# Kernel optimization log

Hardware: AMD Instinct MI355X
Metric: run time of the kernel (lower is better)

## Reference

```python
import jax, jax.numpy as jnp
import numpy as np

N = 100000
E = 3200000
F_IN = 512
H = 16
C = 40


def gcn_conv(x, edge_index, W, b, num_nodes):
    """PyG GCNConv: y = D^{-1/2} (A + I) D^{-1/2} (x @ W) + b.
    edge_index: [2, E] int, row=source, col=target; self-loops added here."""
    # transform first (small hidden dim keeps message traffic low)
    h = x @ W  # [N, out]
    loops = jnp.arange(num_nodes, dtype=edge_index.dtype)
    row = jnp.concatenate([edge_index[0], loops])
    col = jnp.concatenate([edge_index[1], loops])
    deg = jax.ops.segment_sum(jnp.ones_like(col, dtype=h.dtype), col,
                              num_segments=num_nodes)  # in-degree incl. self-loop
    dinv = jnp.where(deg > 0, jax.lax.rsqrt(deg), 0.0)
    norm = dinv[row] * dinv[col]  # [E+N]
    msgs = h[row] * norm[:, None]  # gather + scale, [E+N, out]
    out = jax.ops.segment_sum(msgs, col, num_segments=num_nodes)  # scatter-add
    return out + b


def setup_inputs() -> dict:
    key = jax.random.key(0)
    k1, k2, k3, k4, k5, k6 = jax.random.split(key, 6)
    x = jax.random.normal(k1, (N, F_IN), dtype=jnp.float32)
    edge_index = jax.random.randint(k2, (2, E), 0, N, dtype=jnp.int64)
    s1 = 1.0 / np.sqrt(F_IN)
    s2 = 1.0 / np.sqrt(H)
    W1 = jax.random.uniform(k3, (F_IN, H), jnp.float32, -s1, s1)
    b1 = jnp.zeros((H,), jnp.float32)
    W2 = jax.random.uniform(k4, (H, C), jnp.float32, -s2, s2)
    b2 = jnp.zeros((C,), jnp.float32)
    return {"x": x, "edge_index": edge_index, "W1": W1, "b1": b1,
            "W2": W2, "b2": b2}


def reference(x, edge_index, W1, b1, W2, b2):
    h = gcn_conv(x, edge_index, W1, b1, N)
    h = jax.nn.relu(h)
    # F.dropout(training=self.training): inference mode -> identity
    h = gcn_conv(h, edge_index, W2, b2, N)
    return jax.nn.log_softmax(h, axis=1)
```

## Files before the change

### kernel.cpp

```cpp
#include <hip/hip_runtime.h>

#define NN 100000
#define EE 3200000
#define FIN 512
#define HH 16
#define CC 40

#define SHIFT 9
#define BNODES 512
#define NB 196
#define CAP 20480
#define CH 2048
#define TC ((EE + CH - 1) / CH)
#define GB2 ((NN + 63) / 64)

__device__ __forceinline__ float bf2f(unsigned short u) {
    return __uint_as_float(((unsigned)u) << 16);
}
__device__ __forceinline__ unsigned short f2bf(float f) {
    unsigned b = __float_as_uint(f);
    return (unsigned short)((b + 0x7FFF + ((b >> 16) & 1)) >> 16);
}

__global__ void k_bin(const int* __restrict__ ei, int* __restrict__ head,
                      int* __restrict__ deg, unsigned* __restrict__ pairs) {
    __shared__ int h[NB];
    __shared__ int gbase[NB];
    __shared__ int lhead[NB];
    __shared__ unsigned esrc[CH];
    __shared__ unsigned edst[CH];
    __shared__ int is64_s;
    int t = threadIdx.x;
    if (t < 64) {
        int nz = (ei[2 * t + 1] != 0) ? 1 : 0;
        unsigned long long m = __ballot(nz);
        if (t == 0) is64_s = (m == 0ULL) ? 1 : 0;
    }
    for (int i = t; i < NB; i += 256) { h[i] = 0; lhead[i] = 0; }
    __syncthreads();
    int is64 = is64_s;
    int e0 = blockIdx.x * CH, e1 = min(EE, e0 + CH);
    for (int e = e0 + t; e < e1; e += 256) {
        int src = is64 ? ei[2 * e] : ei[e];
        int dst = is64 ? ei[2 * (EE + e)] : ei[EE + e];
        esrc[e - e0] = (unsigned)src;
        edst[e - e0] = (unsigned)dst;
        atomicAdd(&h[dst >> SHIFT], 1);
        atomicAdd(&deg[dst], 1);
    }
    __syncthreads();
    for (int i = t; i < NB; i += 256)
        gbase[i] = h[i] ? atomicAdd(&head[i], h[i]) : 0;
    __syncthreads();
    int n = e1 - e0;
    for (int j = t; j < n; j += 256) {
        unsigned src = esrc[j];
        unsigned dst = edst[j];
        int b = (int)(dst >> SHIFT);
        int p = gbase[b] + atomicAdd(&lhead[b], 1);
        pairs[(size_t)b * CAP + p] = ((dst & (BNODES - 1)) << 17) | src;
    }
}

__global__ void __launch_bounds__(256) k_buildgemm(
        const unsigned* __restrict__ pairs, const int* __restrict__ head,
        int* __restrict__ ptr, int* __restrict__ pend,
        float* __restrict__ dinv, int* __restrict__ srcs,
        const float* __restrict__ x, const float* __restrict__ W1,
        const int* __restrict__ deg, unsigned short* __restrict__ g1) {
    __shared__ float red[4][64][17];
    int t = threadIdx.x;
    if (blockIdx.x < NB) {
        int* h   = (int*)red;
        int* lex = (int*)red + BNODES;
        int* wsm = (int*)red + 2 * BNODES;
        int b = blockIdx.x, lane = t & 63, wid = t >> 6;
        int node0 = b << SHIFT;
        int p0 = b * CAP;
        int cnt = head[b];
        for (int i = t; i < BNODES; i += 256) h[i] = 0;
        __syncthreads();
        for (int p = t; p < cnt; p += 256) atomicAdd(&h[pairs[p0 + p] >> 17], 1);
        __syncthreads();
        int a0 = h[2 * t], a1 = h[2 * t + 1];
        int s = a0 + a1;
        int v = s;
#pragma unroll
        for (int off = 1; off < 64; off <<= 1) {
            int u = __shfl_up(v, off);
            if (lane >= off) v += u;
        }
        if (lane == 63) wsm[wid] = v;
        __syncthreads();
        int add = 0;
        for (int w = 0; w < wid; ++w) add += wsm[w];
        int incl = v + add;
        int e0 = incl - s;
        lex[2 * t] = e0;
        lex[2 * t + 1] = e0 + a0;
        __syncthreads();
        for (int i = t; i < BNODES; i += 256) {
            int n = node0 + i;
            if (n < NN) {
                int st = p0 + lex[i];
                ptr[n] = st;
                pend[n] = st + h[i];
                dinv[n] = rsqrtf((float)(h[i] + 1));
            }
        }
        __syncthreads();
        for (int p = t; p < cnt; p += 256) {
            unsigned w = pairs[p0 + p];
            int pos = p0 + atomicAdd(&lex[w >> 17], 1);
            srcs[pos] = (int)(w & 0x1FFFF);
        }
    } else {
        int kq = __builtin_amdgcn_readfirstlane(t >> 6);
        int n = t & 63;
        int base = (blockIdx.x - NB) * 64;
        int nc = min(base + n, NN - 1);
        const float4* xr = reinterpret_cast<const float4*>(
            x + (size_t)nc * FIN + kq * 128);
        const float* wb = W1 + kq * 128 * HH;
        float acc[HH];
#pragma unroll
        for (int f = 0; f < HH; ++f) acc[f] = 0.f;
#pragma unroll 2
        for (int i = 0; i < 32; ++i) {
            float4 xv = xr[i];
            const float* wr = wb + i * 4 * HH;
#pragma unroll
            for (int f = 0; f < HH; ++f) acc[f] = fmaf(xv.x, wr[f], acc[f]);
#pragma unroll
            for (int f = 0; f < HH; ++f) acc[f] = fmaf(xv.y, wr[HH + f], acc[f]);
#pragma unroll
            for (int f = 0; f < HH; ++f) acc[f] = fmaf(xv.z, wr[2 * HH + f], acc[f]);
#pragma unroll
            for (int f = 0; f < HH; ++f) acc[f] = fmaf(xv.w, wr[3 * HH + f], acc[f]);
        }
#pragma unroll
        for (int f = 0; f < HH; ++f) red[kq][n][f] = acc[f];
        __syncthreads();
        int g = t >> 6;
        int f0 = g * 4;
        float r0 = red[0][n][f0]     + red[1][n][f0]     + red[2][n][f0]     + red[3][n][f0];
        float r1 = red[0][n][f0 + 1] + red[1][n][f0 + 1] + red[2][n][f0 + 1] + red[3][n][f0 + 1];
        float r2 = red[0][n][f0 + 2] + red[1][n][f0 + 2] + red[2][n][f0 + 2] + red[3][n][f0 + 2];
        float r3 = red[0][n][f0 + 3] + red[1][n][f0 + 3] + red[2][n][f0 + 3] + red[3][n][f0 + 3];
        int node = base + n;
        if (node < NN) {
            float di = rsqrtf((float)(deg[node] + 1));
            ushort4 o;
            o.x = f2bf(r0 * di);
            o.y = f2bf(r1 * di);
            o.z = f2bf(r2 * di);
            o.w = f2bf(r3 * di);
            reinterpret_cast<ushort4*>(g1)[node * 4 + g] = o;
        }
    }
}

__global__ void k_agg1(const unsigned short* __restrict__ g1, const int* __restrict__ ptr,
                       const int* __restrict__ pend, const int* __restrict__ srcs,
                       const float* __restrict__ dinv, const float* __restrict__ b1,
                       unsigned short* __restrict__ g2h) {
    int gt = blockIdx.x * blockDim.x + threadIdx.x;
    int node = gt >> 2, q = gt & 3;
    if (node >= NN) return;
    const ushort4* G = reinterpret_cast<const ushort4*>(g1);
    ushort4 sv = G[node * 4 + q];
    float ax = bf2f(sv.x), ay = bf2f(sv.y), az = bf2f(sv.z), aw = bf2f(sv.w);
    float bx = 0.f, by = 0.f, bz = 0.f, bw = 0.f;
    float cx = 0.f, cy = 0.f, cz = 0.f, cw = 0.f;
    float dx = 0.f, dy = 0.f, dz = 0.f, dw = 0.f;
    int e = ptr[node], e1 = pend[node];
    for (; e + 3 < e1; e += 4) {
        int s0 = srcs[e], s1 = srcs[e + 1], s2 = srcs[e + 2], s3 = srcs[e + 3];
        ushort4 v0 = G[s0 * 4 + q];
        ushort4 v1 = G[s1 * 4 + q];
        ushort4 v2 = G[s2 * 4 + q];
        ushort4 v3 = G[s3 * 4 + q];
        ax += bf2f(v0.x); ay += bf2f(v0.y); az += bf2f(v0.z); aw += bf2f(v0.w);
        bx += bf2f(v1.x); by += bf2f(v1.y); bz += bf2f(v1.z); bw += bf2f(v1.w);
        cx += bf2f(v2.x); cy += bf2f(v2.y); cz += bf2f(v2.z); cw += bf2f(v2.w);
        dx += bf2f(v3.x); dy += bf2f(v3.y); dz += bf2f(v3.z); dw += bf2f(v3.w);
    }
    for (; e < e1; ++e) {
        ushort4 v = G[srcs[e] * 4 + q];
        ax += bf2f(v.x); ay += bf2f(v.y); az += bf2f(v.z); aw += bf2f(v.w);
    }
    ax += bx + cx + dx;
    ay += by + cy + dy;
    az += bz + cz + dz;
    aw += bw + cw + dw;
    float di = dinv[node];
    const float4 bb = reinterpret_cast<const float4*>(b1)[q];
    ushort4 r;
    r.x = f2bf(fmaxf(fmaf(di, ax, bb.x), 0.f) * di);
    r.y = f2bf(fmaxf(fmaf(di, ay, bb.y), 0.f) * di);
    r.z = f2bf(fmaxf(fmaf(di, az, bb.z), 0.f) * di);
    r.w = f2bf(fmaxf(fmaf(di, aw, bb.w), 0.f) * di);
    reinterpret_cast<ushort4*>(g2h)[node * 4 + q] = r;
}

__global__ void __launch_bounds__(256) k_agg2out(
        const unsigned short* __restrict__ g2h, const int* __restrict__ ptr,
        const int* __restrict__ pend, const int* __restrict__ srcs,
        const float* __restrict__ dinv, const float* __restrict__ W2,
        const float* __restrict__ b2, float* __restrict__ out) {
    __shared__ float w2s[HH * 41];
    __shared__ float b2s[CC];
    int t = threadIdx.x;
    for (int i = t; i < HH * CC; i += 256) w2s[(i / CC) * 41 + (i % CC)] = W2[i];
    if (t < CC) b2s[t] = b2[t];
    __syncthreads();
    int gt = blockIdx.x * blockDim.x + t;
    int node = gt >> 2, q = gt & 3;
    if (node >= NN) return;
    const ushort4* G = reinterpret_cast<const ushort4*>(g2h);
    ushort4 sv = G[node * 4 + q];
    float ax = bf2f(sv.x), ay = bf2f(sv.y), az = bf2f(sv.z), aw = bf2f(sv.w);
    float bx = 0.f, by = 0.f, bz = 0.f, bw = 0.f;
    float cx = 0.f, cy = 0.f, cz = 0.f, cw = 0.f;
    float dx = 0.f, dy = 0.f, dz = 0.f, dw = 0.f;
    int e = ptr[node], e1 = pend[node];
    for (; e + 3 < e1; e += 4) {
        int s0 = srcs[e], s1 = srcs[e + 1], s2 = srcs[e + 2], s3 = srcs[e + 3];
        ushort4 v0 = G[s0 * 4 + q];
        ushort4 v1 = G[s1 * 4 + q];
        ushort4 v2 = G[s2 * 4 + q];
        ushort4 v3 = G[s3 * 4 + q];
        ax += bf2f(v0.x); ay += bf2f(v0.y); az += bf2f(v0.z); aw += bf2f(v0.w);
        bx += bf2f(v1.x); by += bf2f(v1.y); bz += bf2f(v1.z); bw += bf2f(v1.w);
        cx += bf2f(v2.x); cy += bf2f(v2.y); cz += bf2f(v2.z); cw += bf2f(v2.w);
        dx += bf2f(v3.x); dy += bf2f(v3.y); dz += bf2f(v3.z); dw += bf2f(v3.w);
    }
    for (; e < e1; ++e) {
        ushort4 v = G[srcs[e] * 4 + q];
        ax += bf2f(v.x); ay += bf2f(v.y); az += bf2f(v.z); aw += bf2f(v.w);
    }
    ax += bx + cx + dx;
    ay += by + cy + dy;
    az += bz + cz + dz;
    aw += bw + cw + dw;
    const float* w0 = w2s + (4 * q + 0) * 41;
    const float* w1 = w2s + (4 * q + 1) * 41;
    const float* w2r = w2s + (4 * q + 2) * 41;
    const float* w3 = w2s + (4 * q + 3) * 41;
    float y[CC];
#pragma unroll
    for (int c = 0; c < CC; ++c)
        y[c] = fmaf(ax, w0[c], fmaf(ay, w1[c], fmaf(az, w2r[c], aw * w3[c])));
#pragma unroll
    for (int c = 0; c < CC; ++c) {
        y[c] += __shfl_xor(y[c], 1);
        y[c] += __shfl_xor(y[c], 2);
    }
    float di = dinv[node];
    float m = -3.0e38f;
#pragma unroll
    for (int c = 0; c < CC; ++c) {
        y[c] = fmaf(di, y[c], b2s[c]);
        m = fmaxf(m, y[c]);
    }
    float ssum = 0.f;
#pragma unroll
    for (int c = 0; c < CC; ++c) ssum += expf(y[c] - m);
    float l = logf(ssum) + m;
    float ov[10];
#pragma unroll
    for (int c = 0; c < CC; ++c) {
        if ((c / 10) == q) ov[c % 10] = y[c] - l;
    }
    float2* o2 = reinterpret_cast<float2*>(out + (size_t)node * CC + 10 * q);
#pragma unroll
    for (int i = 0; i < 5; ++i) o2[i] = make_float2(ov[2 * i], ov[2 * i + 1]);
}

extern "C" void kernel_launch(void* const* d_in, const int* in_sizes, int n_in,
                              void* d_out, int out_size, void* d_ws, size_t ws_size,
                              hipStream_t stream) {
    const float* x  = (const float*)d_in[0];
    const int*   ei = (const int*)d_in[1];
    const float* W1 = (const float*)d_in[2];
    const float* b1 = (const float*)d_in[3];
    const float* W2 = (const float*)d_in[4];
    const float* b2 = (const float*)d_in[5];
    float* out = (float*)d_out;

    char* w = (char*)d_ws;
    auto alloc = [&](size_t bytes) {
        char* p = w;
        w += (bytes + 255) & ~(size_t)255;
        return p;
    };
    int*            head  = (int*)alloc((size_t)(NB + NN) * 4);
    int*            deg   = head + NB;
    int*            ptr   = (int*)alloc((size_t)NN * 4);
    int*            pend  = (int*)alloc((size_t)NN * 4);
    float*          dinv  = (float*)alloc((size_t)NN * 4);
    unsigned*       pairs = (unsigned*)alloc((size_t)NB * CAP * 4);
    int*            srcs  = (int*)alloc((size_t)NB * CAP * 4);
    unsigned short* g1    = (unsigned short*)alloc((size_t)NN * HH * 2);
    unsigned short* g2h   = (unsigned short*)alloc((size_t)NN * HH * 2);

    hipMemsetAsync(head, 0, (size_t)(NB + NN) * sizeof(int), stream);
    k_bin<<<TC, 256, 0, stream>>>(ei, head, deg, pairs);
    k_buildgemm<<<NB + GB2, 256, 0, stream>>>(pairs, head, ptr, pend, dinv, srcs,
                                              x, W1, deg, g1);
    int nt = NN * 4;
    k_agg1<<<(nt + 255) / 256, 256, 0, stream>>>(g1, ptr, pend, srcs, dinv, b1, g2h);
    k_agg2out<<<(nt + 255) / 256, 256, 0, stream>>>(g2h, ptr, pend, srcs, dinv,
                                                    W2, b2, out);
}
```

Before: 570.6 us.

## Drop global degree atomics in binning; scale GEMM output in separate pass

Removes the per-edge global atomicAdd on the degree array from the binning kernel, relying on dinv computed from the per-bucket histograms in the build kernel. Edge endpoints are kept in registers instead of shared memory staging. Because dinv is only available after the build phase, the GEMM now writes unscaled fp32 results and a new small kernel applies dinv and converts to bf16. This trades 3.2M scattered global atomics and a large memset for an extra 6.4MB write, a re-read of that buffer, and one extra launch.

```diff
diff --git a/kernel.cpp b/kernel.cpp
--- a/kernel.cpp
+++ b/kernel.cpp
@@ -12,6 +12,7 @@
 #define CAP 20480
 #define CH 2048
 #define TC ((EE + CH - 1) / CH)
+#define GB ((NN * 4 + 255) / 256)
 #define GB2 ((NN + 63) / 64)
 
 __device__ __forceinline__ float bf2f(unsigned short u) {
@@ -23,12 +24,10 @@
 }
 
 __global__ void k_bin(const int* __restrict__ ei, int* __restrict__ head,
-                      int* __restrict__ deg, unsigned* __restrict__ pairs) {
+                      unsigned* __restrict__ pairs) {
     __shared__ int h[NB];
     __shared__ int gbase[NB];
     __shared__ int lhead[NB];
-    __shared__ unsigned esrc[CH];
-    __shared__ unsigned edst[CH];
     __shared__ int is64_s;
     int t = threadIdx.x;
     if (t < 64) {
@@ -39,26 +38,29 @@
     for (int i = t; i < NB; i += 256) { h[i] = 0; lhead[i] = 0; }
     __syncthreads();
     int is64 = is64_s;
-    int e0 = blockIdx.x * CH, e1 = min(EE, e0 + CH);
-    for (int e = e0 + t; e < e1; e += 256) {
-        int src = is64 ? ei[2 * e] : ei[e];
-        int dst = is64 ? ei[2 * (EE + e)] : ei[EE + e];
-        esrc[e - e0] = (unsigned)src;
-        edst[e - e0] = (unsigned)dst;
-        atomicAdd(&h[dst >> SHIFT], 1);
-        atomicAdd(&deg[dst], 1);
+    int e0 = blockIdx.x * CH;
+    unsigned es[8], ed[8];
+#pragma unroll
+    for (int j = 0; j < 8; ++j) {
+        int e = e0 + j * 256 + t;
+        if (e < EE) {
+            es[j] = (unsigned)(is64 ? ei[2 * e] : ei[e]);
+            ed[j] = (unsigned)(is64 ? ei[2 * (EE + e)] : ei[EE + e]);
+            atomicAdd(&h[ed[j] >> SHIFT], 1);
+        }
     }
     __syncthreads();
     for (int i = t; i < NB; i += 256)
         gbase[i] = h[i] ? atomicAdd(&head[i], h[i]) : 0;
     __syncthreads();
-    int n = e1 - e0;
-    for (int j = t; j < n; j += 256) {
-        unsigned src = esrc[j];
-        unsigned dst = edst[j];
-        int b = (int)(dst >> SHIFT);
-        int p = gbase[b] + atomicAdd(&lhead[b], 1);
-        pairs[(size_t)b * CAP + p] = ((dst & (BNODES - 1)) << 17) | src;
+#pragma unroll
+    for (int j = 0; j < 8; ++j) {
+        int e = e0 + j * 256 + t;
+        if (e < EE) {
+            int b = (int)(ed[j] >> SHIFT);
+            int p = gbase[b] + atomicAdd(&lhead[b], 1);
+            pairs[(size_t)b * CAP + p] = ((ed[j] & (BNODES - 1)) << 17) | es[j];
+        }
     }
 }
 
@@ -67,7 +69,7 @@
         int* __restrict__ ptr, int* __restrict__ pend,
         float* __restrict__ dinv, int* __restrict__ srcs,
         const float* __restrict__ x, const float* __restrict__ W1,
-        const int* __restrict__ deg, unsigned short* __restrict__ g1) {
+        float* __restrict__ g1f) {
     __shared__ float red[4][64][17];
     int t = threadIdx.x;
     if (blockIdx.x < NB) {
@@ -148,16 +150,25 @@
         float r2 = red[0][n][f0 + 2] + red[1][n][f0 + 2] + red[2][n][f0 + 2] + red[3][n][f0 + 2];
         float r3 = red[0][n][f0 + 3] + red[1][n][f0 + 3] + red[2][n][f0 + 3] + red[3][n][f0 + 3];
         int node = base + n;
-        if (node < NN) {
-            float di = rsqrtf((float)(deg[node] + 1));
-            ushort4 o;
-            o.x = f2bf(r0 * di);
-            o.y = f2bf(r1 * di);
-            o.z = f2bf(r2 * di);
-            o.w = f2bf(r3 * di);
-            reinterpret_cast<ushort4*>(g1)[node * 4 + g] = o;
-        }
-    }
+        if (node < NN)
+            reinterpret_cast<float4*>(g1f)[node * 4 + g] =
+                make_float4(r0, r1, r2, r3);
+    }
+}
+
+__global__ void k_scale(const float* __restrict__ g1f, const float* __restrict__ dinv,
+                        unsigned short* __restrict__ g1) {
+    int gt = blockIdx.x * 256 + threadIdx.x;
+    int node = gt >> 2, q = gt & 3;
+    if (node >= NN) return;
+    float di = dinv[node];
+    float4 v = reinterpret_cast<const float4*>(g1f)[node * 4 + q];
+    ushort4 o;
+    o.x = f2bf(v.x * di);
+    o.y = f2bf(v.y * di);
+    o.z = f2bf(v.z * di);
+    o.w = f2bf(v.w * di);
+    reinterpret_cast<ushort4*>(g1)[node * 4 + q] = o;
 }
 
 __global__ void k_agg1(const unsigned short* __restrict__ g1, const int* __restrict__ ptr,
@@ -294,20 +305,21 @@
         w += (bytes + 255) & ~(size_t)255;
         return p;
     };
-    int*            head  = (int*)alloc((size_t)(NB + NN) * 4);
-    int*            deg   = head + NB;
+    int*            head  = (int*)alloc((size_t)NB * 4);
     int*            ptr   = (int*)alloc((size_t)NN * 4);
     int*            pend  = (int*)alloc((size_t)NN * 4);
     float*          dinv  = (float*)alloc((size_t)NN * 4);
     unsigned*       pairs = (unsigned*)alloc((size_t)NB * CAP * 4);
     int*            srcs  = (int*)alloc((size_t)NB * CAP * 4);
+    float*          g1f   = (float*)alloc((size_t)NN * HH * 4);
     unsigned short* g1    = (unsigned short*)alloc((size_t)NN * HH * 2);
     unsigned short* g2h   = (unsigned short*)alloc((size_t)NN * HH * 2);
 
-    hipMemsetAsync(head, 0, (size_t)(NB + NN) * sizeof(int), stream);
-    k_bin<<<TC, 256, 0, stream>>>(ei, head, deg, pairs);
+    hipMemsetAsync(head, 0, (size_t)NB * sizeof(int), stream);
+    k_bin<<<TC, 256, 0, stream>>>(ei, head, pairs);
     k_buildgemm<<<NB + GB2, 256, 0, stream>>>(pairs, head, ptr, pend, dinv, srcs,
-                                              x, W1, deg, g1);
+                                              x, W1, g1f);
+    k_scale<<<GB, 256, 0, stream>>>(g1f, dinv, g1);
     int nt = NN * 4;
     k_agg1<<<(nt + 255) / 256, 256, 0, stream>>>(g1, ptr, pend, srcs, dinv, b1, g2h);
     k_agg2out<<<(nt + 255) / 256, 256, 0, stream>>>(g2h, ptr, pend, srcs, dinv,
```

Result: faster. 468.3 us (-17.9%).
